# Kernel optimization log

Hardware: AMD Instinct MI355X
Metric: run time of the kernel (lower is better)

Reference implementation:

```python
import jax, jax.numpy as jnp
import numpy as np

N = 50000          # num nodes
DEG = 16           # fixed degree (uniform CSR)
E = N * DEG        # num edges
R = 8              # num relations
IN = 128
HID = 128
OUT = 40
BN_EPS = 1e-5


def setup_inputs() -> dict:
    key = jax.random.key(0)
    k = jax.random.split(key, 5)
    x = jax.random.normal(k[0], (N, IN), jnp.float32)
    # glorot-ish init for per-relation weights
    W1 = jax.random.normal(k[1], (R, IN, HID), jnp.float32) * (2.0 / (IN + HID)) ** 0.5
    W2 = jax.random.normal(k[2], (R, HID, OUT), jnp.float32) * (2.0 / (HID + OUT)) ** 0.5
    ptr = jnp.arange(N + 1, dtype=jnp.int32) * DEG            # CSR row offsets
    idx = jax.random.randint(k[3], (E,), 0, N, jnp.int32)     # neighbor (src) ids
    edge_types = jax.random.randint(k[4], (E,), 0, R, jnp.int32)
    return {
        "x": x, "W1": W1, "W2": W2,
        "bn_gamma": jnp.ones((HID,), jnp.float32),
        "bn_beta": jnp.zeros((HID,), jnp.float32),
        "bn_mean": jnp.zeros((HID,), jnp.float32),
        "bn_var": jnp.ones((HID,), jnp.float32),
        "ptr": ptr, "idx": idx, "edge_types": edge_types,
    }


def _rgcn_layer(h, W, ptr, idx, edge_types):
    # RGCNOP: out[i] = sum_{e in [ptr[i],ptr[i+1])} x[idx[e]] @ W[etype[e]]
    # Efficient form: transform every node by every relation once, then gather
    # the (src, etype) pair per edge and scatter-add into destinations.
    xr = jnp.einsum('nd,rdh->nrh', h, W)             # [N, R, H]
    msgs = xr[idx, edge_types]                       # [E, H] irregular gather
    deg = ptr[1:] - ptr[:-1]                         # [N]
    dst = jnp.repeat(jnp.arange(ptr.shape[0] - 1, dtype=jnp.int32), deg,
                     total_repeat_length=idx.shape[0])
    agg = jax.ops.segment_sum(msgs, dst, num_segments=ptr.shape[0] - 1)
    return agg / deg[:, None].astype(agg.dtype)      # degree normalization


def reference(x, W1, W2, bn_gamma, bn_beta, bn_mean, bn_var, ptr, idx, edge_types):
    h = _rgcn_layer(x, W1, ptr, idx, edge_types)
    # BatchNorm1d in eval mode (history_size=0, dropout inactive)
    h = (h - bn_mean) * jax.lax.rsqrt(bn_var + BN_EPS) * bn_gamma + bn_beta
    h = jax.nn.relu(h)
    h = _rgcn_layer(h, W2, ptr, idx, edge_types)
    return jax.nn.log_softmax(h, axis=-1)
```

## Files before the change

kernel.cpp:

```cpp
#include <hip/hip_runtime.h>
#include <hip/hip_fp8.h>
#include <math.h>

typedef __attribute__((ext_vector_type(8))) short bf16x8;
typedef __attribute__((ext_vector_type(4))) float f32x4;

constexpr int kN   = 50000;
constexpr int kIn  = 128;
constexpr int kHid = 128;
constexpr int kOut = 40;
constexpr int kNT  = 16;
constexpr int kLds = 1032;
constexpr float kBnEps = 1e-5f;

constexpr size_t kOffW2hi = 262144;
constexpr size_t kOffW2z  = 360448;
constexpr size_t kOffXb   = 524288;
constexpr size_t kOffBig  = 13324288;
constexpr size_t kZBytes  = (size_t)kN * 512;

__device__ inline float bf2f(ushort s) { return __uint_as_float(((uint)s) << 16); }

__device__ __forceinline__ ushort f2bf(float x) {
    uint u = __float_as_uint(x);
    u += 0x7FFFu + ((u >> 16) & 1u);
    return (ushort)(u >> 16);
}

__device__ __forceinline__ uint cvtpk(float a, float b) {
    uint r;
    asm("v_cvt_pk_bf16_f32 %0, %1, %2" : "=v"(r) : "v"(a), "v"(b));
    return r;
}

__device__ __forceinline__ uchar f2fp8(float x) {
    __hip_fp8_e4m3 v(x);
    return *(uchar*)&v;
}
__device__ __forceinline__ float fp82f(uchar b) {
    __hip_fp8_e4m3 v;
    *(uchar*)&v = b;
    return (float)v;
}

#define RD(V, J) __builtin_amdgcn_readlane((V), (J))

__device__ __forceinline__ void pack_unit(const float* __restrict__ W,
                                          ushort* __restrict__ dst,
                                          int N, int frag, int lane)
{
    const int kt = frag & 31;
    const int nt = frag >> 5;
    const int n  = nt * 16 + (lane & 15);
    const int q  = lane >> 4;
    float f[8];
    #pragma unroll
    for (int j = 0; j < 8; ++j) {
        const int k = kt * 32 + q * 8 + j;
        f[j] = (n < N) ? W[(size_t)k * N + n] : 0.f;
    }
    const size_t o = ((size_t)frag * 64 + lane) * 8;
    *(uint4*)&dst[o] = make_uint4(cvtpk(f[0], f[1]), cvtpk(f[2], f[3]),
                                  cvtpk(f[4], f[5]), cvtpk(f[6], f[7]));
}

__global__ __launch_bounds__(256)
void prep(const float* __restrict__ x,  ushort* __restrict__ xb,
          const float* __restrict__ W1, ushort* __restrict__ W1hi,
          const float* __restrict__ W2, ushort* __restrict__ W2hi,
          ushort* __restrict__ W2z, int useZ)
{
    const int b   = blockIdx.x;
    const int tid = threadIdx.x;
    if (b < 3125) {
        const size_t i = ((size_t)b * 256 + tid) * 8;
        const float4 v0 = *(const float4*)&x[i];
        const float4 v1 = *(const float4*)&x[i + 4];
        *(uint4*)&xb[i] = make_uint4(cvtpk(v0.x, v0.y), cvtpk(v0.z, v0.w),
                                     cvtpk(v1.x, v1.y), cvtpk(v1.z, v1.w));
    } else if (b < 3125 + 64) {
        pack_unit(W1, W1hi, kHid, (b - 3125) * 4 + (tid >> 6), tid & 63);
    } else if (b < 3213) {
        const int frag = (b - 3189) * 4 + (tid >> 6);
        if (frag < 96) pack_unit(W2, W2hi, kOut, frag, tid & 63);
    } else if (useZ) {
        const int frag = (b - 3213) * 4 + (tid >> 6);
        const int kt   = frag & 3;
        const int nt   = frag >> 2;
        const int lane = tid & 63;
        const int c    = nt * 16 + (lane & 15);
        const int r    = c >> 6;
        const int o    = c & 63;
        const int q    = lane >> 4;
        float f[8];
        #pragma unroll
        for (int j = 0; j < 8; ++j) {
            const int k = kt * 32 + q * 8 + j;
            f[j] = (o < kOut) ? W2[((size_t)r * kHid + k) * kOut + o] : 0.f;
        }
        const size_t of = ((size_t)frag * 64 + lane) * 8;
        *(uint4*)&W2z[of] = make_uint4(cvtpk(f[0], f[1]), cvtpk(f[2], f[3]),
                                       cvtpk(f[4], f[5]), cvtpk(f[6], f[7]));
    }
}

__device__ __forceinline__ void stage_fast(const char* fb, int vi, char* msW,
                                           int hOff, int lane)
{
    const int b = (lane & 7) * 16;
    #pragma unroll
    for (int u = 0; u < 4; ++u) {
        const int e   = u * 8 + (lane >> 3);
        const int src = __shfl(vi, e, 64);
        const uint4 v = *(const uint4*)(fb + (((size_t)(uint)src) << 8) + hOff + b);
        *(uint4*)(msW + e * 128 + (b ^ (u << 5))) = v;
    }
}

__device__ __forceinline__ void stage_slow(const char* fb,
                                           const int* __restrict__ idx,
                                           int p0, int p1, int deg0, int deg1,
                                           char* msW, int hOff, int lane)
{
    const int l31 = lane & 31;
    if (lane < 32) {
        for (int e = 0; e < 32; ++e) {
            const bool eok = (e < 16) ? (e < deg0) : ((e - 16) < deg1);
            uint val = 0;
            if (eok) {
                const int g = (e < 16) ? (p0 + e) : (p1 + (e - 16));
                const int s = idx[g];
                val = *(const uint*)(fb + (((size_t)(uint)s) << 8) + hOff + l31 * 4);
            }
            *(uint*)(msW + e * 128 + ((l31 * 4) ^ (((e >> 3) & 3) << 5))) = val;
        }
    }
}

__device__ __forceinline__ bf16x8 readB(const char* msW, int q, int m, int ntL)
{
    const char* ap = msW + q * 1024 + 2 * m + (((ntL ^ q) & 3) << 5);
    bf16x8 b;
    #pragma unroll
    for (int j = 0; j < 8; ++j) b[j] = *(const short*)(ap + j * 128);
    return b;
}

__device__ __forceinline__ void mfma_store(bf16x8 aS, bf16x8 bb, int fbase,
                                           int ntL, int w, int q, int m,
                                           ushort (*aggHi)[kLds])
{
    f32x4 z = {0.f, 0.f, 0.f, 0.f};
    const f32x4 d = __builtin_amdgcn_mfma_f32_16x16x32_bf16(aS, bb, z, 0, 0, 0);
    ushort* dst = &aggHi[2 * w + (q >> 1)][0];
    const int fcol = fbase + ntL * 16 + m;
    const int rb   = (q & 1) * 4;
    dst[(rb + 0) * 128 + fcol] = f2bf(d[0]);
    dst[(rb + 1) * 128 + fcol] = f2bf(d[1]);
    dst[(rb + 2) * 128 + fcol] = f2bf(d[2]);
    dst[(rb + 3) * 128 + fcol] = f2bf(d[3]);
}

__device__ __forceinline__ void phaseA_mfma(const ushort* __restrict__ feat,
                                            const int* __restrict__ ptr,
                                            const int* __restrict__ idx,
                                            const int* __restrict__ etype,
                                            int base, ushort (*aggHi)[kLds],
                                            char* msgs)
{
    const int lane = threadIdx.x & 63;
    const int w    = threadIdx.x >> 6;
    const int m    = lane & 15;
    const int q    = lane >> 4;
    const char* fb = (const char*)feat;

    const int node0 = base + 2 * w;
    const int p0 = ptr[node0];
    const int p1 = ptr[node0 + 1];
    const int p2 = ptr[node0 + 2];
    const int deg0 = p1 - p0, deg1 = p2 - p1;
    const bool fast = (deg0 == 16) && (deg1 == 16);

    const int vi = idx  [p0 + (lane & 31)];
    const int ve = etype[p0 + (lane & 31)];

    char* msW = msgs + w * 4096;

    int code;
    if (fast) {
        code = (((lane & 31) >> 4) << 3) | ve;
    } else {
        const int l31 = lane & 31;
        const bool eok = (l31 < 16) ? (l31 < deg0) : ((l31 - 16) < deg1);
        code = eok ? (((l31 >> 4) << 3) | ve) : 0xFF;
    }

    bf16x8 aS;
    #pragma unroll
    for (int j = 0; j < 8; ++j) {
        const int cj = __shfl(code, q * 8 + j, 64);
        aS[j] = (cj == m) ? (short)0x3F80 : (short)0;
    }

    if (fast) stage_fast(fb, vi, msW, 0, lane);
    else      stage_slow(fb, idx, p0, p1, deg0, deg1, msW, 0, lane);
    const bf16x8 b0 = readB(msW, q, m, 0);
    const bf16x8 b1 = readB(msW, q, m, 1);
    const bf16x8 b2 = readB(msW, q, m, 2);
    const bf16x8 b3 = readB(msW, q, m, 3);

    if (fast) stage_fast(fb, vi, msW, 128, lane);
    else      stage_slow(fb, idx, p0, p1, deg0, deg1, msW, 128, lane);

    mfma_store(aS, b0, 0, 0, w, q, m, aggHi);
    mfma_store(aS, b1, 0, 1, w, q, m, aggHi);
    mfma_store(aS, b2, 0, 2, w, q, m, aggHi);
    mfma_store(aS, b3, 0, 3, w, q, m, aggHi);

    const bf16x8 c0 = readB(msW, q, m, 0);
    const bf16x8 c1 = readB(msW, q, m, 1);
    const bf16x8 c2 = readB(msW, q, m, 2);
    const bf16x8 c3 = readB(msW, q, m, 3);
    mfma_store(aS, c0, 64, 0, w, q, m, aggHi);
    mfma_store(aS, c1, 64, 1, w, q, m, aggHi);
    mfma_store(aS, c2, 64, 2, w, q, m, aggHi);
    mfma_store(aS, c3, 64, 3, w, q, m, aggHi);
}

__global__ __launch_bounds__(512, 4)
void rgcn_layer1(const ushort* __restrict__ xb,
                 const ushort* __restrict__ W1hi,
                 const ushort* __restrict__ W2z,
                 const float* __restrict__ gamma, const float* __restrict__ beta,
                 const float* __restrict__ mean,  const float* __restrict__ var,
                 const int* __restrict__ ptr, const int* __restrict__ idx,
                 const int* __restrict__ etype,
                 ushort* __restrict__ h1b, uchar* __restrict__ zbuf, int useZ)
{
    __shared__ ushort aggHi[kNT][kLds];
    __shared__ __align__(16) char msgs[8 * 4096];
    const int tid  = threadIdx.x;
    const int base = blockIdx.x * kNT;

    phaseA_mfma(xb, ptr, idx, etype, base, aggHi, msgs);
    __syncthreads();

    const int lane = tid & 63;
    const int wid  = tid >> 6;
    const int m    = lane & 15;
    const int q    = lane >> 4;

    const bf16x8* Bh = (const bf16x8*)W1hi + (size_t)wid * 32 * 64 + lane;
    f32x4 acc = {0.f, 0.f, 0.f, 0.f};

    #pragma unroll 4
    for (int kt = 0; kt < 32; ++kt) {
        const bf16x8 ah = *(const bf16x8*)&aggHi[m][kt * 32 + q * 8];
        const bf16x8 bh = Bh[(size_t)kt * 64];
        acc = __builtin_amdgcn_mfma_f32_16x16x32_bf16(ah, bh, acc, 0, 0, 0);
    }

    const int c = wid * 16 + m;
    const float g  = gamma[c] * rsqrtf(var[c] + kBnEps);
    const float mu = mean[c];
    const float bt = beta[c];
    float v[4];
    #pragma unroll
    for (int i = 0; i < 4; ++i) {
        const int node = base + q * 4 + i;
        const float invdeg = 1.0f / (float)(ptr[node + 1] - ptr[node]);
        v[i] = fmaxf((acc[i] * invdeg - mu) * g + bt, 0.f);
    }
    const uint p01 = cvtpk(v[0], v[1]);
    const uint p23 = cvtpk(v[2], v[3]);

    if (useZ) {
        ushort (*h1lds)[136] = (ushort (*)[136])(msgs + 16768);
        h1lds[q * 4 + 0][c] = (ushort)(p01 & 0xFFFFu);
        h1lds[q * 4 + 1][c] = (ushort)(p01 >> 16);
        h1lds[q * 4 + 2][c] = (ushort)(p23 & 0xFFFFu);
        h1lds[q * 4 + 3][c] = (ushort)(p23 >> 16);
        __syncthreads();

        ushort (*zlds)[524] = (ushort (*)[524])msgs;
        const bf16x8* B2 = (const bf16x8*)W2z;
        #pragma unroll
        for (int t = 0; t < 4; ++t) {
            const int nt = wid * 4 + t;
            f32x4 a2 = {0.f, 0.f, 0.f, 0.f};
            #pragma unroll
            for (int kt2 = 0; kt2 < 4; ++kt2) {
                const bf16x8 ah2 = *(const bf16x8*)&h1lds[m][kt2 * 32 + q * 8];
                const bf16x8 bh2 = B2[(size_t)(nt * 4 + kt2) * 64 + lane];
                a2 = __builtin_amdgcn_mfma_f32_16x16x32_bf16(ah2, bh2, a2, 0, 0, 0);
            }
            zlds[q * 4 + 0][nt * 16 + m] = f2bf(a2[0]);
            zlds[q * 4 + 1][nt * 16 + m] = f2bf(a2[1]);
            zlds[q * 4 + 2][nt * 16 + m] = f2bf(a2[2]);
            zlds[q * 4 + 3][nt * 16 + m] = f2bf(a2[3]);
        }
        __syncthreads();

        const int row = tid >> 5;
        const int cs  = (tid & 31) * 16;
        alignas(16) uchar ob[16];
        #pragma unroll
        for (int jj = 0; jj < 16; ++jj)
            ob[jj] = f2fp8(bf2f(zlds[row][cs + jj]));
        uchar* zp = zbuf + ((size_t)(base + row)) * 512 + cs;
        *(uint4*)zp = *(const uint4*)ob;
    } else {
        const int n0 = base + q * 4;
        h1b[(size_t)(n0 + 0) * kHid + c] = (ushort)(p01 & 0xFFFFu);
        h1b[(size_t)(n0 + 1) * kHid + c] = (ushort)(p01 >> 16);
        h1b[(size_t)(n0 + 2) * kHid + c] = (ushort)(p23 & 0xFFFFu);
        h1b[(size_t)(n0 + 3) * kHid + c] = (ushort)(p23 >> 16);
    }
}

__global__ __launch_bounds__(512, 4)
void rgcn_layer2(const ushort* __restrict__ h1b,
                 const ushort* __restrict__ W2hi,
                 const int* __restrict__ ptr, const int* __restrict__ idx,
                 const int* __restrict__ etype,
                 float* __restrict__ out)
{
    __shared__ ushort aggHi[kNT][kLds];
    __shared__ __align__(16) char msgs[8 * 4096];
    __shared__ float logits[kNT][48];
    const int tid  = threadIdx.x;
    const int base = blockIdx.x * kNT;

    phaseA_mfma(h1b, ptr, idx, etype, base, aggHi, msgs);
    __syncthreads();

    const int lane = tid & 63;
    const int wid  = tid >> 6;
    const int m    = lane & 15;
    const int q    = lane >> 4;

    if (wid < 3) {
        const bf16x8* Bh = (const bf16x8*)W2hi + (size_t)wid * 32 * 64 + lane;
        f32x4 acc = {0.f, 0.f, 0.f, 0.f};
        #pragma unroll 4
        for (int kt = 0; kt < 32; ++kt) {
            const bf16x8 ah = *(const bf16x8*)&aggHi[m][kt * 32 + q * 8];
            const bf16x8 bh = Bh[(size_t)kt * 64];
            acc = __builtin_amdgcn_mfma_f32_16x16x32_bf16(ah, bh, acc, 0, 0, 0);
        }
        const int n = wid * 16 + m;
        if (n < kOut) {
            #pragma unroll
            for (int i = 0; i < 4; ++i) {
                const int node = base + q * 4 + i;
                const float invdeg = 1.0f / (float)(ptr[node + 1] - ptr[node]);
                logits[q * 4 + i][n] = acc[i] * invdeg;
            }
        }
    }
    __syncthreads();

    #pragma unroll
    for (int i = 0; i < 2; ++i) {
        const int nrow = wid * 2 + i;
        const int node = base + nrow;
        const float v = (lane < kOut) ? logits[nrow][lane] : -INFINITY;
        float mx = v;
        #pragma unroll
        for (int off = 32; off > 0; off >>= 1)
            mx = fmaxf(mx, __shfl_xor(mx, off, 64));
        float s = (lane < kOut) ? __expf(v - mx) : 0.f;
        #pragma unroll
        for (int off = 32; off > 0; off >>= 1)
            s += __shfl_xor(s, off, 64);
        if (lane < kOut)
            out[(size_t)node * kOut + lane] = v - mx - __logf(s);
    }
}

__global__ __launch_bounds__(256)
void rgcn_layer2z(const uchar* __restrict__ z8,
                  const int* __restrict__ ptr, const int* __restrict__ idx,
                  const int* __restrict__ etype,
                  float* __restrict__ out)
{
    const int lane = threadIdx.x & 63;
    const int wv   = threadIdx.x >> 6;
    const int n0   = blockIdx.x * 16 + wv * 4;

    const int p0 = ptr[n0];
    const int d0 = ptr[n0 + 1] - p0;
    const int d1 = ptr[n0 + 2] - ptr[n0 + 1];
    const int d2 = ptr[n0 + 3] - ptr[n0 + 2];
    const int d3 = ptr[n0 + 4] - ptr[n0 + 3];
    const bool fast = (d0 == 16) & (d1 == 16) & (d2 == 16) & (d3 == 16);

    int vi = 0, ve = 0;
    if (fast) { vi = idx[p0 + lane]; ve = etype[p0 + lane]; }

    #pragma unroll
    for (int t = 0; t < 4; ++t) {
        const int node = n0 + t;
        float acc = 0.f;
        float invdeg;
        if (fast) {
            invdeg = 0.0625f;
            #pragma unroll
            for (int j = 0; j < 16; ++j) {
                const int e = t * 16 + j;
                const int s = RD(vi, e);
                const int r = RD(ve, e);
                acc += fp82f(z8[(size_t)(uint)s * 512 + (r << 6) + lane]);
            }
        } else {
            const int pa = ptr[node], pb = ptr[node + 1];
            invdeg = 1.0f / (float)(pb - pa);
            for (int e = pa; e < pb; ++e) {
                const int s = __builtin_amdgcn_readfirstlane(idx[e]);
                const int r = __builtin_amdgcn_readfirstlane(etype[e]);
                acc += fp82f(z8[(size_t)(uint)s * 512 + (r << 6) + lane]);
            }
        }
        const float v = (lane < kOut) ? acc * invdeg : -INFINITY;
        float mx = v;
        #pragma unroll
        for (int off = 32; off > 0; off >>= 1)
            mx = fmaxf(mx, __shfl_xor(mx, off, 64));
        float s2 = (lane < kOut) ? __expf(v - mx) : 0.f;
        #pragma unroll
        for (int off = 32; off > 0; off >>= 1)
            s2 += __shfl_xor(s2, off, 64);
        if (lane < kOut)
            out[(size_t)node * kOut + lane] = v - mx - __logf(s2);
    }
}

extern "C" void kernel_launch(void* const* d_in, const int* in_sizes, int n_in,
                              void* d_out, int out_size, void* d_ws, size_t ws_size,
                              hipStream_t stream)
{
    const float* x     = (const float*)d_in[0];
    const float* W1    = (const float*)d_in[1];
    const float* W2    = (const float*)d_in[2];
    const float* gamma = (const float*)d_in[3];
    const float* beta  = (const float*)d_in[4];
    const float* mean  = (const float*)d_in[5];
    const float* var   = (const float*)d_in[6];
    const int*   ptr   = (const int*)d_in[7];
    const int*   idx   = (const int*)d_in[8];
    const int*   et    = (const int*)d_in[9];
    float*       out   = (float*)d_out;

    char* ws = (char*)d_ws;
    ushort* W1hi = (ushort*)ws;
    ushort* W2hi = (ushort*)(ws + kOffW2hi);
    ushort* W2z  = (ushort*)(ws + kOffW2z);
    ushort* xb   = (ushort*)(ws + kOffXb);
    ushort* h1b  = (ushort*)(ws + kOffBig);
    uchar*  z8   = (uchar*)(ws + kOffBig);

    const int useZ = (ws_size >= kOffBig + kZBytes) ? 1 : 0;

    prep<<<dim3(3245), dim3(256), 0, stream>>>(x, xb, W1, W1hi, W2, W2hi,
                                               W2z, useZ);

    dim3 grid(kN / kNT), block(512);
    rgcn_layer1<<<grid, block, 0, stream>>>(xb, W1hi, W2z, gamma, beta, mean,
                                            var, ptr, idx, et, h1b, z8, useZ);
    if (useZ) {
        rgcn_layer2z<<<dim3(kN / 16), dim3(256), 0, stream>>>(z8, ptr, idx,
                                                              et, out);
    } else {
        rgcn_layer2<<<grid, block, 0, stream>>>(h1b, W2hi, ptr, idx, et, out);
    }
}
```

Baseline: 185.2 us.

## Vectorize layer-2 gather: 16 lanes per node, 4 fp8 values per lane

```diff
diff --git a/kernel.cpp b/kernel.cpp
--- a/kernel.cpp
+++ b/kernel.cpp
@@ -387,6 +387,9 @@
     const int lane = threadIdx.x & 63;
     const int wv   = threadIdx.x >> 6;
     const int n0   = blockIdx.x * 16 + wv * 4;
+    const int g    = lane >> 4;
+    const int c4   = (lane & 15) * 4;
+    const int node = n0 + g;
 
     const int p0 = ptr[n0];
     const int d0 = ptr[n0 + 1] - p0;
@@ -395,43 +398,56 @@
     const int d3 = ptr[n0 + 4] - ptr[n0 + 3];
     const bool fast = (d0 == 16) & (d1 == 16) & (d2 == 16) & (d3 == 16);
 
-    int vi = 0, ve = 0;
-    if (fast) { vi = idx[p0 + lane]; ve = etype[p0 + lane]; }
-
-    #pragma unroll
-    for (int t = 0; t < 4; ++t) {
-        const int node = n0 + t;
-        float acc = 0.f;
-        float invdeg;
-        if (fast) {
-            invdeg = 0.0625f;
-            #pragma unroll
-            for (int j = 0; j < 16; ++j) {
-                const int e = t * 16 + j;
-                const int s = RD(vi, e);
-                const int r = RD(ve, e);
-                acc += fp82f(z8[(size_t)(uint)s * 512 + (r << 6) + lane]);
-            }
-        } else {
-            const int pa = ptr[node], pb = ptr[node + 1];
-            invdeg = 1.0f / (float)(pb - pa);
-            for (int e = pa; e < pb; ++e) {
-                const int s = __builtin_amdgcn_readfirstlane(idx[e]);
-                const int r = __builtin_amdgcn_readfirstlane(etype[e]);
-                acc += fp82f(z8[(size_t)(uint)s * 512 + (r << 6) + lane]);
-            }
-        }
-        const float v = (lane < kOut) ? acc * invdeg : -INFINITY;
-        float mx = v;
-        #pragma unroll
-        for (int off = 32; off > 0; off >>= 1)
-            mx = fmaxf(mx, __shfl_xor(mx, off, 64));
-        float s2 = (lane < kOut) ? __expf(v - mx) : 0.f;
-        #pragma unroll
-        for (int off = 32; off > 0; off >>= 1)
-            s2 += __shfl_xor(s2, off, 64);
-        if (lane < kOut)
-            out[(size_t)node * kOut + lane] = v - mx - __logf(s2);
+    float a0 = 0.f, a1 = 0.f, a2 = 0.f, a3 = 0.f;
+    float invdeg;
+
+    if (fast) {
+        invdeg = 0.0625f;
+        const int vi = idx  [p0 + lane];
+        const int ve = etype[p0 + lane];
+        #pragma unroll
+        for (int j = 0; j < 16; ++j) {
+            const int E = g * 16 + j;
+            const int s = __shfl(vi, E, 64);
+            const int r = __shfl(ve, E, 64);
+            const uint off = (uint)s * 512u + ((uint)r << 6) + (uint)c4;
+            const uint v = *(const uint*)(z8 + off);
+            a0 += fp82f((uchar)(v));
+            a1 += fp82f((uchar)(v >> 8));
+            a2 += fp82f((uchar)(v >> 16));
+            a3 += fp82f((uchar)(v >> 24));
+        }
+    } else {
+        const int pa = ptr[node], pb = ptr[node + 1];
+        invdeg = 1.0f / (float)(pb - pa);
+        for (int e = pa; e < pb; ++e) {
+            const int s = idx[e];
+            const int r = etype[e];
+            const uint off = (uint)s * 512u + ((uint)r << 6) + (uint)c4;
+            const uint v = *(const uint*)(z8 + off);
+            a0 += fp82f((uchar)(v));
+            a1 += fp82f((uchar)(v >> 8));
+            a2 += fp82f((uchar)(v >> 16));
+            a3 += fp82f((uchar)(v >> 24));
+        }
+    }
+
+    const bool valid = (lane & 15) < 10;
+    const float v0 = a0 * invdeg, v1 = a1 * invdeg;
+    const float v2 = a2 * invdeg, v3 = a3 * invdeg;
+    float mx = valid ? fmaxf(fmaxf(v0, v1), fmaxf(v2, v3)) : -INFINITY;
+    #pragma unroll
+    for (int off = 8; off > 0; off >>= 1)
+        mx = fmaxf(mx, __shfl_xor(mx, off, 64));
+    float sm = valid ? (__expf(v0 - mx) + __expf(v1 - mx) +
+                        __expf(v2 - mx) + __expf(v3 - mx)) : 0.f;
+    #pragma unroll
+    for (int off = 8; off > 0; off >>= 1)
+        sm += __shfl_xor(sm, off, 64);
+    if (valid) {
+        const float lg = mx + __logf(sm);
+        const float4 o4 = make_float4(v0 - lg, v1 - lg, v2 - lg, v3 - lg);
+        *(float4*)&out[(size_t)node * kOut + c4] = o4;
     }
 }
 
```

After: 182.1 us. No clear change (-1.7%).
